# Kernel optimization log

Measured on AMD Instinct MI355X. Metric: run time of the kernel, lower is better.

Reference implementation:

```python
import jax, jax.numpy as jnp
import numpy as np

D_MODEL = 768
N_HEADS = 8
HEAD_DIM = D_MODEL // N_HEADS
B, S, A = 8, 8192, 512


def setup_inputs() -> dict:
    key = jax.random.key(0)
    ks = jax.random.split(key, 12)
    hidden_states = jax.random.normal(ks[0], (B, S, D_MODEL), dtype=jnp.float32)
    # unique anchors per batch element (scatter with duplicates is ill-defined)
    anchor_indices = jax.vmap(lambda k: jax.random.permutation(k, S)[:A])(
        jax.random.split(ks[1], B)).astype(jnp.int64)
    std = 1.0 / np.sqrt(D_MODEL)
    def lin(kw, kb):
        w = jax.random.uniform(kw, (D_MODEL, D_MODEL), jnp.float32, -std, std)
        b = jax.random.uniform(kb, (D_MODEL,), jnp.float32, -std, std)
        return w, b
    wq, bq = lin(ks[2], ks[3])
    wk, bk = lin(ks[4], ks[5])
    wv, bv = lin(ks[6], ks[7])
    wo, bo = lin(ks[8], ks[9])
    ln_g = jnp.ones((D_MODEL,), jnp.float32)
    ln_b = jnp.zeros((D_MODEL,), jnp.float32)
    return dict(hidden_states=hidden_states, anchor_indices=anchor_indices,
                ln_g=ln_g, ln_b=ln_b, wq=wq, bq=bq, wk=wk, bk=bk,
                wv=wv, bv=bv, wo=wo, bo=bo)


def reference(hidden_states, anchor_indices, ln_g, ln_b, wq, bq, wk, bk, wv, bv, wo, bo):
    batch, seq_len, d_model = hidden_states.shape
    n_anchors = anchor_indices.shape[1]
    # gather anchor tokens: (B, A, D)
    anchor_hidden = jnp.take_along_axis(hidden_states, anchor_indices[..., None], axis=1)
    # LayerNorm (eps=1e-5, matching nn.LayerNorm default)
    mu = jnp.mean(anchor_hidden, axis=-1, keepdims=True)
    var = jnp.var(anchor_hidden, axis=-1, keepdims=True)
    x = (anchor_hidden - mu) * jax.lax.rsqrt(var + 1e-5) * ln_g + ln_b
    # QKV projections -> (B, H, A, Hd)
    def heads(y):
        return y.reshape(batch, n_anchors, N_HEADS, HEAD_DIM).transpose(0, 2, 1, 3)
    q = heads(x @ wq.T + bq)
    k = heads(x @ wk.T + bk)
    v = heads(x @ wv.T + bv)
    scale = 1.0 / np.sqrt(HEAD_DIM)
    scores = jnp.einsum('bhad,bhed->bhae', q, k) * scale  # (B,H,A,A)
    attn = jax.nn.softmax(scores, axis=-1)  # dropout is identity in eval
    out = jnp.einsum('bhae,bhed->bhad', attn, v)
    out = out.transpose(0, 2, 1, 3).reshape(batch, n_anchors, d_model)
    out = out @ wo.T + bo
    # scatter back into zeros at anchor positions
    batch_idx = jnp.arange(batch)[:, None]
    output = jnp.zeros_like(hidden_states).at[batch_idx, anchor_indices].set(out)
    return output
```

## Files before the change

kernel.cpp:

```cpp
#include <hip/hip_runtime.h>

#define DM 768
#define NHEAD 8
#define HDIM 96
#define NB 8
#define SEQ 8192
#define NA 512
#define MROW (NB*NA)
#define NQKV (3*DM)
#define QBLK 32
#define ATTNB 1024
#define PFILLB 256

typedef __attribute__((ext_vector_type(4))) float f32x4;
typedef __attribute__((ext_vector_type(8))) short s16x8;

static __device__ __forceinline__ unsigned short f2bf(float x) {
  unsigned int u = __float_as_uint(x);
  u += 0x7fffu + ((u >> 16) & 1u);
  return (unsigned short)(u >> 16);
}

static __device__ __forceinline__ void gld_lds16(const void* g, void* l) {
  __builtin_amdgcn_global_load_lds(
      (const __attribute__((address_space(1))) unsigned int*)g,
      (__attribute__((address_space(3))) unsigned int*)l, 16, 0, 0);
}

__global__ __launch_bounds__(512) void prologue(
    const float* __restrict__ hs, const int* __restrict__ anc,
    const float* __restrict__ gam, const float* __restrict__ bet,
    const float* __restrict__ wq, const float* __restrict__ wk,
    const float* __restrict__ wv, const float* __restrict__ wo,
    unsigned short* __restrict__ xh,
    unsigned short* __restrict__ w1h, unsigned short* __restrict__ woh,
    f32x4* __restrict__ fillp, int fstart, int fend)
{
  const int bid = blockIdx.x;
  const int t = threadIdx.x;
  if (bid < 512) {
    const int w = t >> 6, lane = t & 63;
    const int r = bid * 8 + w;
    const int b = r >> 9, a = r & (NA - 1);
    const int idx = anc[b * NA + a];
    const float4* src4 = reinterpret_cast<const float4*>(hs + ((size_t)b * SEQ + idx) * DM);
    float4 e[3];
    float s = 0.f, ss = 0.f;
    #pragma unroll
    for (int p = 0; p < 3; ++p) {
      e[p] = src4[lane * 3 + p];
      s  += e[p].x + e[p].y + e[p].z + e[p].w;
      ss += e[p].x*e[p].x + e[p].y*e[p].y + e[p].z*e[p].z + e[p].w*e[p].w;
    }
    #pragma unroll
    for (int o = 1; o < 64; o <<= 1) { s += __shfl_xor(s, o); ss += __shfl_xor(ss, o); }
    const float mu = s * (1.f / DM);
    const float var = ss * (1.f / DM) - mu * mu;
    const float rstd = rsqrtf(var + 1e-5f);
    uint2* dst = reinterpret_cast<uint2*>(xh + (size_t)r * DM);
    const float4* g4 = reinterpret_cast<const float4*>(gam);
    const float4* b4 = reinterpret_cast<const float4*>(bet);
    #pragma unroll
    for (int p = 0; p < 3; ++p) {
      const float4 gv = g4[lane * 3 + p], bv = b4[lane * 3 + p];
      const float y0 = (e[p].x - mu) * rstd * gv.x + bv.x;
      const float y1 = (e[p].y - mu) * rstd * gv.y + bv.y;
      const float y2 = (e[p].z - mu) * rstd * gv.z + bv.z;
      const float y3 = (e[p].w - mu) * rstd * gv.w + bv.w;
      uint2 pk;
      pk.x = (unsigned)f2bf(y0) | ((unsigned)f2bf(y1) << 16);
      pk.y = (unsigned)f2bf(y2) | ((unsigned)f2bf(y3) << 16);
      dst[lane * 3 + p] = pk;
    }
  } else if (bid < 800) {
    const int base = (bid - 512) * 2048;
    const int T1_4 = (NQKV * DM) / 4;
    const int TW_4 = (DM * DM) / 4;
    #pragma unroll
    for (int rep = 0; rep < 4; ++rep) {
      const int i = base + rep * 512 + t;
      float4 v; unsigned short* dh; int e4;
      if (i < T1_4) {
        v = (i < TW_4) ? reinterpret_cast<const float4*>(wq)[i]
          : (i < 2*TW_4) ? reinterpret_cast<const float4*>(wk)[i - TW_4]
                         : reinterpret_cast<const float4*>(wv)[i - 2*TW_4];
        dh = w1h; e4 = i;
      } else {
        const int j = i - T1_4;
        v = reinterpret_cast<const float4*>(wo)[j];
        dh = woh; e4 = j;
      }
      uint2 ph;
      ph.x = (unsigned)f2bf(v.x) | ((unsigned)f2bf(v.y) << 16);
      ph.y = (unsigned)f2bf(v.z) | ((unsigned)f2bf(v.w) << 16);
      reinterpret_cast<uint2*>(dh)[e4] = ph;
    }
  } else {
    const f32x4 z = {0.f, 0.f, 0.f, 0.f};
    int i = fstart + (bid - 800) * 512 + t;
    for (; i < fend; i += PFILLB * 512) __builtin_nontemporal_store(z, fillp + i);
  }
}

template<int EPI, int BM, int BN, int NCOMP, int GCOLS>
__global__ __launch_bounds__(256, 4) void gemm_t(
    const unsigned short* __restrict__ Ah,
    const unsigned short* __restrict__ Bh,
    const float* __restrict__ biasq, const float* __restrict__ biask, const float* __restrict__ biasv,
    unsigned short* __restrict__ qh,
    unsigned short* __restrict__ kh,
    unsigned short* __restrict__ vh,
    const float* __restrict__ biaso, const int* __restrict__ anc,
    float* __restrict__ outp,
    f32x4* __restrict__ fillp, int fstart, int fend)
{
  constexpr int MI = BM / 32, NJ = BN / 32;
  __shared__ unsigned short sA[BM * 64], sB[BN * 64];
  const int bidx = blockIdx.x;
  const int tid = threadIdx.x, lane = tid & 63, w = tid >> 6;
  const int wr = w >> 1, wc = w & 1;
  const unsigned int wg = ((unsigned)bidx & 7) * (NCOMP >> 3) + ((unsigned)bidx >> 3);
  const int m0 = (int)(wg / GCOLS) * BM, n0 = (int)(wg % GCOLS) * BN;
  const int rsel = lane & 15, kg = lane >> 4;
  f32x4 acc[MI][NJ] = {};

  for (int k0 = 0; k0 < DM; k0 += 64) {
    __syncthreads();
    #pragma unroll
    for (int c = 0; c < (BM + BN) / 32; ++c) {
      const int gg = c * 256 + w * 64;
      const int g = gg + lane;
      if (g < BM * 8) {
        const int row = g >> 3, slot = g & 7;
        const int kk = k0 + ((slot ^ (row & 7)) << 3);
        gld_lds16(Ah + (size_t)(m0 + row) * DM + kk, sA + gg * 8);
      } else {
        const int g2 = g - BM * 8;
        const int row = g2 >> 3, slot = g2 & 7;
        const int kk = k0 + ((slot ^ (row & 7)) << 3);
        gld_lds16(Bh + (size_t)(n0 + row) * DM + kk, sB + (gg - BM * 8) * 8);
      }
    }
    __syncthreads();
    #pragma unroll
    for (int s = 0; s < 2; ++s) {
      s16x8 af[MI], bf[NJ];
      #pragma unroll
      for (int i = 0; i < MI; ++i) {
        const int row = wr * (MI * 16) + i * 16 + rsel;
        const int as = (((s << 2) | kg) ^ (row & 7));
        af[i] = *reinterpret_cast<const s16x8*>(sA + row * 64 + as * 8);
      }
      #pragma unroll
      for (int j = 0; j < NJ; ++j) {
        const int col = wc * (NJ * 16) + j * 16 + rsel;
        const int bs = (((s << 2) | kg) ^ (col & 7));
        bf[j] = *reinterpret_cast<const s16x8*>(sB + col * 64 + bs * 8);
      }
      #pragma unroll
      for (int i = 0; i < MI; ++i)
        #pragma unroll
        for (int j = 0; j < NJ; ++j)
          acc[i][j] = __builtin_amdgcn_mfma_f32_16x16x32_bf16(af[i], bf[j], acc[i][j], 0, 0, 0);
    }
  }

  #pragma unroll
  for (int i = 0; i < MI; ++i)
    #pragma unroll
    for (int j = 0; j < NJ; ++j)
      #pragma unroll
      for (int r = 0; r < 4; ++r) {
        const int row = m0 + wr * (MI * 16) + i * 16 + kg * 4 + r;
        const int col = n0 + wc * (NJ * 16) + j * 16 + rsel;
        const float v = acc[i][j][r];
        const int b = row >> 9, a = row & (NA - 1);
        if (EPI == 1) {
          const int sec = (col >= 2 * DM) ? 2 : (col >= DM ? 1 : 0);
          const int f = col - sec * DM;
          const int hh = f / HDIM, d = f - hh * HDIM;
          const float* bp = (sec == 0) ? biasq : (sec == 1) ? biask : biasv;
          const float val = v + bp[f];
          const int bhh = b * NHEAD + hh;
          if (sec == 0) {
            const size_t o = ((size_t)bhh * NA + a) * HDIM + d; qh[o] = f2bf(val);
          } else if (sec == 1) {
            const size_t o = ((size_t)bhh * NA + a) * HDIM + d; kh[o] = f2bf(val);
          } else {
            const size_t o = ((size_t)bhh * HDIM + d) * NA + a; vh[o] = f2bf(val);
          }
        } else {
          const int sidx = anc[b * NA + a];
          outp[((size_t)b * SEQ + sidx) * DM + col] = v + biaso[col];
        }
      }

  if (EPI == 1) {
    const f32x4 z = {0.f, 0.f, 0.f, 0.f};
    for (int i = fstart + bidx * 256 + tid; i < fend; i += NCOMP * 256)
      __builtin_nontemporal_store(z, fillp + i);
  }
}

__global__ __launch_bounds__(512, 4) void attn_fused(
    const unsigned short* __restrict__ qh,
    const unsigned short* __restrict__ kh,
    const unsigned short* __restrict__ vh,
    unsigned short* __restrict__ oh,
    f32x4* __restrict__ fillp, int fstart, int fend)
{
  __shared__ unsigned int S[QBLK * 512];
  __shared__ float rsum_lds[QBLK];
  const int blk = blockIdx.x;
  const int xcd = blk & 7, slot = blk >> 3;
  const int qt = slot & 15, bh = (slot >> 4) * 8 + xcd;
  const int b = bh >> 3, h = bh & 7;
  const int tid = threadIdx.x, lane = tid & 63, w = tid >> 6;
  const int rt = w & 1, ctq = w >> 1;
  const int rsel = lane & 15, kg = lane >> 4;
  const int q0 = qt * QBLK;

  s16x8 qf[3];
  {
    const size_t qrow = (size_t)bh * NA + q0 + rt * 16 + rsel;
    const unsigned short* qp = qh + qrow * HDIM + kg * 8;
    #pragma unroll
    for (int kc = 0; kc < 3; ++kc)
      qf[kc] = *reinterpret_cast<const s16x8*>(qp + kc * 32);
  }
  const float scale = 0.10206207261596575f;
  const unsigned short* kb_h = kh + (size_t)bh * NA * HDIM + (size_t)rsel * HDIM + kg * 8;

  #pragma unroll
  for (int ct2 = 0; ct2 < 8; ++ct2) {
    const int ct = ctq * 8 + ct2;
    f32x4 acc = {0.f, 0.f, 0.f, 0.f};
    const unsigned short* kp = kb_h + (size_t)(ct * 16) * HDIM;
    s16x8 kf0 = *reinterpret_cast<const s16x8*>(kp);
    s16x8 kf1 = *reinterpret_cast<const s16x8*>(kp + 32);
    s16x8 kf2 = *reinterpret_cast<const s16x8*>(kp + 64);
    acc = __builtin_amdgcn_mfma_f32_16x16x32_bf16(qf[0], kf0, acc, 0, 0, 0);
    acc = __builtin_amdgcn_mfma_f32_16x16x32_bf16(qf[1], kf1, acc, 0, 0, 0);
    acc = __builtin_amdgcn_mfma_f32_16x16x32_bf16(qf[2], kf2, acc, 0, 0, 0);
    #pragma unroll
    for (int r = 0; r < 4; ++r) {
      int row = rt * 16 + kg * 4 + r;
      int col = ct * 16 + rsel;
      S[row * 512 + (col ^ ((row & 7) << 2))] = __float_as_uint(acc[r] * scale);
    }
  }
  __syncthreads();

  {
    const int row = w * 4 + (lane >> 4);
    const int sub = lane & 15;
    const int srow = (row & 7) << 2;
    unsigned int* rowp = &S[row * 512];
    float sum = 0.f;
    #pragma unroll
    for (int i = 0; i < 8; ++i) {
      int c = sub * 4 + i * 64;
      uint4 u = *reinterpret_cast<const uint4*>(rowp + (c ^ srow));
      float p0 = __expf(__uint_as_float(u.x));
      float p1 = __expf(__uint_as_float(u.y));
      float p2 = __expf(__uint_as_float(u.z));
      float p3 = __expf(__uint_as_float(u.w));
      sum += p0 + p1 + p2 + p3;
      uint4 pk;
      pk.x = ((unsigned)f2bf(p0)) << 16;
      pk.y = ((unsigned)f2bf(p1)) << 16;
      pk.z = ((unsigned)f2bf(p2)) << 16;
      pk.w = ((unsigned)f2bf(p3)) << 16;
      *reinterpret_cast<uint4*>(rowp + (c ^ srow)) = pk;
    }
    sum += __shfl_xor(sum, 1);
    sum += __shfl_xor(sum, 2);
    sum += __shfl_xor(sum, 4);
    sum += __shfl_xor(sum, 8);
    if (sub == 0) rsum_lds[row] = 1.f / sum;
  }
  __syncthreads();

  const unsigned short* vb_h = vh + (size_t)bh * HDIM * NA + (size_t)rsel * NA + kg * 8;
  for (int task = w; task < 12; task += 8) {
    const int nt = task % 6, rt2 = task / 6;
    f32x4 acc = {0.f, 0.f, 0.f, 0.f};
    const int row = rt2 * 16 + rsel;
    const int srow = (row & 7) << 2;
    const unsigned int* rowp = &S[row * 512];
    const unsigned short* vp = vb_h + (size_t)(nt * 16) * NA;
    #pragma unroll
    for (int kc = 0; kc < 16; ++kc) {
      int c = kc * 32 + kg * 8;
      s16x8 vfh = *reinterpret_cast<const s16x8*>(vp + kc * 32);
      uint4 ua = *reinterpret_cast<const uint4*>(rowp + ((c) ^ srow));
      uint4 ub = *reinterpret_cast<const uint4*>(rowp + ((c + 4) ^ srow));
      s16x8 ph;
      ph[0] = (short)(ua.x >> 16); ph[1] = (short)(ua.y >> 16);
      ph[2] = (short)(ua.z >> 16); ph[3] = (short)(ua.w >> 16);
      ph[4] = (short)(ub.x >> 16); ph[5] = (short)(ub.y >> 16);
      ph[6] = (short)(ub.z >> 16); ph[7] = (short)(ub.w >> 16);
      acc = __builtin_amdgcn_mfma_f32_16x16x32_bf16(ph, vfh, acc, 0, 0, 0);
    }
    #pragma unroll
    for (int r = 0; r < 4; ++r) {
      const float rinv = rsum_lds[rt2 * 16 + kg * 4 + r];
      const int rowg = b * NA + q0 + rt2 * 16 + kg * 4 + r;
      size_t o = (size_t)rowg * DM + h * HDIM + nt * 16 + rsel;
      oh[o] = f2bf(acc[r] * rinv);
    }
  }

  {
    const f32x4 z = {0.f, 0.f, 0.f, 0.f};
    for (int i = fstart + blk * 512 + tid; i < fend; i += ATTNB * 512)
      __builtin_nontemporal_store(z, fillp + i);
  }
}

extern "C" void kernel_launch(void* const* d_in, const int* in_sizes, int n_in,
                              void* d_out, int out_size, void* d_ws, size_t ws_size,
                              hipStream_t stream)
{
  const float* hs   = (const float*)d_in[0];
  const int*   anc  = (const int*)d_in[1];
  const float* ln_g = (const float*)d_in[2];
  const float* ln_b = (const float*)d_in[3];
  const float* wq = (const float*)d_in[4];
  const float* bq = (const float*)d_in[5];
  const float* wk = (const float*)d_in[6];
  const float* bk = (const float*)d_in[7];
  const float* wv = (const float*)d_in[8];
  const float* bv = (const float*)d_in[9];
  const float* wo = (const float*)d_in[10];
  const float* bo = (const float*)d_in[11];
  float* outp = (float*)d_out;

  char* ws = (char*)d_ws;
  size_t off = 0;
  auto take = [&](size_t bytes) { char* p = ws + off; off += (bytes + 255) & ~(size_t)255; return p; };
  unsigned short* xh  = (unsigned short*)take((size_t)MROW * DM * 2);
  unsigned short* w1h = (unsigned short*)take((size_t)NQKV * DM * 2);
  unsigned short* woh = (unsigned short*)take((size_t)DM * DM * 2);
  const size_t qkvsz = (size_t)NB * NHEAD * NA * HDIM * 2;
  unsigned short* qhb = (unsigned short*)take(qkvsz);
  unsigned short* khb = (unsigned short*)take(qkvsz);
  unsigned short* vhb = (unsigned short*)take(qkvsz);
  unsigned short* ohb = (unsigned short*)take((size_t)MROW * DM * 2);

  const int n4 = out_size / 4;
  const int f1 = n4 / 4;
  const int f2 = (int)(((long long)n4 * 5) / 8);

  prologue<<<800 + PFILLB, 512, 0, stream>>>(
      hs, anc, ln_g, ln_b, wq, wk, wv, wo, xh, w1h, woh,
      (f32x4*)outp, 0, f1);
  gemm_t<1, 128, 96, 768, 24><<<768, 256, 0, stream>>>(
      xh, w1h, bq, bk, bv, qhb, khb, vhb,
      nullptr, nullptr, nullptr,
      (f32x4*)outp, f1, f2);
  attn_fused<<<ATTNB, 512, 0, stream>>>(
      qhb, khb, vhb, ohb, (f32x4*)outp, f2, n4);
  gemm_t<2, 64, 96, 512, 8><<<512, 256, 0, stream>>>(
      ohb, woh, nullptr, nullptr, nullptr,
      nullptr, nullptr, nullptr,
      bo, anc, outp,
      nullptr, 0, 0);
}
```

Before: 105.1 us.

## Store attention scores as bf16 in LDS and rebalance output zero-fill across kernels

The attention score tile in shared memory now holds bf16 instead of fp32 and uses a re-derived XOR swizzle. This halves LDS footprint and traffic, and lets the PV stage load 8-element fragments directly instead of unpacking two uint4 loads. Rounding scores to bf16 before exp adds some precision loss. The zero-fill of the output is also removed from the prologue and split evenly between the QKV GEMM and attention kernels.

```diff
diff --git a/kernel.cpp b/kernel.cpp
--- a/kernel.cpp
+++ b/kernel.cpp
@@ -10,7 +10,6 @@
 #define NQKV (3*DM)
 #define QBLK 32
 #define ATTNB 1024
-#define PFILLB 256
 
 typedef __attribute__((ext_vector_type(4))) float f32x4;
 typedef __attribute__((ext_vector_type(8))) short s16x8;
@@ -19,6 +18,9 @@
   unsigned int u = __float_as_uint(x);
   u += 0x7fffu + ((u >> 16) & 1u);
   return (unsigned short)(u >> 16);
+}
+static __device__ __forceinline__ float bf2f(unsigned short h) {
+  return __uint_as_float(((unsigned int)h) << 16);
 }
 
 static __device__ __forceinline__ void gld_lds16(const void* g, void* l) {
@@ -33,8 +35,7 @@
     const float* __restrict__ wq, const float* __restrict__ wk,
     const float* __restrict__ wv, const float* __restrict__ wo,
     unsigned short* __restrict__ xh,
-    unsigned short* __restrict__ w1h, unsigned short* __restrict__ woh,
-    f32x4* __restrict__ fillp, int fstart, int fend)
+    unsigned short* __restrict__ w1h, unsigned short* __restrict__ woh)
 {
   const int bid = blockIdx.x;
   const int t = threadIdx.x;
@@ -72,7 +73,7 @@
       pk.y = (unsigned)f2bf(y2) | ((unsigned)f2bf(y3) << 16);
       dst[lane * 3 + p] = pk;
     }
-  } else if (bid < 800) {
+  } else {
     const int base = (bid - 512) * 2048;
     const int T1_4 = (NQKV * DM) / 4;
     const int TW_4 = (DM * DM) / 4;
@@ -95,10 +96,6 @@
       ph.y = (unsigned)f2bf(v.z) | ((unsigned)f2bf(v.w) << 16);
       reinterpret_cast<uint2*>(dh)[e4] = ph;
     }
-  } else {
-    const f32x4 z = {0.f, 0.f, 0.f, 0.f};
-    int i = fstart + (bid - 800) * 512 + t;
-    for (; i < fend; i += PFILLB * 512) __builtin_nontemporal_store(z, fillp + i);
   }
 }
 
@@ -209,7 +206,7 @@
     unsigned short* __restrict__ oh,
     f32x4* __restrict__ fillp, int fstart, int fend)
 {
-  __shared__ unsigned int S[QBLK * 512];
+  __shared__ unsigned short S[QBLK * 512];
   __shared__ float rsum_lds[QBLK];
   const int blk = blockIdx.x;
   const int xcd = blk & 7, slot = blk >> 3;
@@ -244,9 +241,9 @@
     acc = __builtin_amdgcn_mfma_f32_16x16x32_bf16(qf[2], kf2, acc, 0, 0, 0);
     #pragma unroll
     for (int r = 0; r < 4; ++r) {
-      int row = rt * 16 + kg * 4 + r;
-      int col = ct * 16 + rsel;
-      S[row * 512 + (col ^ ((row & 7) << 2))] = __float_as_uint(acc[r] * scale);
+      const int row = rt * 16 + kg * 4 + r;
+      const int col = ct * 16 + rsel;
+      S[row * 512 + (col ^ ((row & 7) << 3))] = f2bf(acc[r] * scale);
     }
   }
   __syncthreads();
@@ -254,24 +251,22 @@
   {
     const int row = w * 4 + (lane >> 4);
     const int sub = lane & 15;
-    const int srow = (row & 7) << 2;
-    unsigned int* rowp = &S[row * 512];
+    const int swz = (row & 7) << 3;
+    unsigned short* rowp = &S[row * 512];
     float sum = 0.f;
     #pragma unroll
-    for (int i = 0; i < 8; ++i) {
-      int c = sub * 4 + i * 64;
-      uint4 u = *reinterpret_cast<const uint4*>(rowp + (c ^ srow));
-      float p0 = __expf(__uint_as_float(u.x));
-      float p1 = __expf(__uint_as_float(u.y));
-      float p2 = __expf(__uint_as_float(u.z));
-      float p3 = __expf(__uint_as_float(u.w));
-      sum += p0 + p1 + p2 + p3;
-      uint4 pk;
-      pk.x = ((unsigned)f2bf(p0)) << 16;
-      pk.y = ((unsigned)f2bf(p1)) << 16;
-      pk.z = ((unsigned)f2bf(p2)) << 16;
-      pk.w = ((unsigned)f2bf(p3)) << 16;
-      *reinterpret_cast<uint4*>(rowp + (c ^ srow)) = pk;
+    for (int i = 0; i < 4; ++i) {
+      const int c = sub * 8 + i * 128;
+      s16x8* slotp = reinterpret_cast<s16x8*>(rowp + (c ^ swz));
+      s16x8 u = *slotp;
+      s16x8 pk;
+      #pragma unroll
+      for (int j = 0; j < 8; ++j) {
+        float p = __expf(bf2f((unsigned short)u[j]));
+        sum += p;
+        pk[j] = (short)f2bf(p);
+      }
+      *slotp = pk;
     }
     sum += __shfl_xor(sum, 1);
     sum += __shfl_xor(sum, 2);
@@ -286,20 +281,14 @@
     const int nt = task % 6, rt2 = task / 6;
     f32x4 acc = {0.f, 0.f, 0.f, 0.f};
     const int row = rt2 * 16 + rsel;
-    const int srow = (row & 7) << 2;
-    const unsigned int* rowp = &S[row * 512];
+    const int swz = (row & 7) << 3;
+    const unsigned short* rowp = &S[row * 512];
     const unsigned short* vp = vb_h + (size_t)(nt * 16) * NA;
     #pragma unroll
     for (int kc = 0; kc < 16; ++kc) {
-      int c = kc * 32 + kg * 8;
+      const int c = kc * 32 + kg * 8;
+      s16x8 ph  = *reinterpret_cast<const s16x8*>(rowp + (c ^ swz));
       s16x8 vfh = *reinterpret_cast<const s16x8*>(vp + kc * 32);
-      uint4 ua = *reinterpret_cast<const uint4*>(rowp + ((c) ^ srow));
-      uint4 ub = *reinterpret_cast<const uint4*>(rowp + ((c + 4) ^ srow));
-      s16x8 ph;
-      ph[0] = (short)(ua.x >> 16); ph[1] = (short)(ua.y >> 16);
-      ph[2] = (short)(ua.z >> 16); ph[3] = (short)(ua.w >> 16);
-      ph[4] = (short)(ub.x >> 16); ph[5] = (short)(ub.y >> 16);
-      ph[6] = (short)(ub.z >> 16); ph[7] = (short)(ub.w >> 16);
       acc = __builtin_amdgcn_mfma_f32_16x16x32_bf16(ph, vfh, acc, 0, 0, 0);
     }
     #pragma unroll
@@ -349,18 +338,16 @@
   unsigned short* ohb = (unsigned short*)take((size_t)MROW * DM * 2);
 
   const int n4 = out_size / 4;
-  const int f1 = n4 / 4;
-  const int f2 = (int)(((long long)n4 * 5) / 8);
-
-  prologue<<<800 + PFILLB, 512, 0, stream>>>(
-      hs, anc, ln_g, ln_b, wq, wk, wv, wo, xh, w1h, woh,
-      (f32x4*)outp, 0, f1);
+  const int fmid = n4 / 2;
+
+  prologue<<<800, 512, 0, stream>>>(
+      hs, anc, ln_g, ln_b, wq, wk, wv, wo, xh, w1h, woh);
   gemm_t<1, 128, 96, 768, 24><<<768, 256, 0, stream>>>(
       xh, w1h, bq, bk, bv, qhb, khb, vhb,
       nullptr, nullptr, nullptr,
-      (f32x4*)outp, f1, f2);
+      (f32x4*)outp, 0, fmid);
   attn_fused<<<ATTNB, 512, 0, stream>>>(
-      qhb, khb, vhb, ohb, (f32x4*)outp, f2, n4);
+      qhb, khb, vhb, ohb, (f32x4*)outp, fmid, n4);
   gemm_t<2, 64, 96, 512, 8><<<512, 256, 0, stream>>>(
       ohb, woh, nullptr, nullptr, nullptr,
       nullptr, nullptr, nullptr,
```

New measurement: 100.9 us. 1.04x faster.
